# Optimization experiments

Measured on AMD Instinct MI355X. Metric: run time of the kernel, lower is better.

The kernel has to match this reference:

```python
import jax, jax.numpy as jnp
import numpy as np

HEADS = 16
DIMS = [64, 64, 64, 64]  # [d_att(Q), d_att(K), d_ff(V), d_ff(G)]
EPS = 1e-4
P_POW = 2


def _cdist(Q, K):
    # Euclidean pairwise distance via the norm expansion, like torch.cdist.
    # Q: [h, b, t, d], K: [h, b, t, d] -> [h, b, t, t]
    q2 = jnp.sum(Q * Q, axis=-1)  # [h, b, t]
    k2 = jnp.sum(K * K, axis=-1)  # [h, b, t]
    qk = jnp.einsum('hbtd,hbsd->hbts', Q, K)
    d2 = q2[..., :, None] + k2[..., None, :] - 2.0 * qk
    return jnp.sqrt(jnp.maximum(d2, 0.0))


def setup_inputs() -> dict:
    key = jax.random.key(0)
    ks = jax.random.split(key, 4)
    b, t, d_in = 2, 2048, 1024
    d_proj = HEADS * sum(DIMS)  # 4096
    X = jax.random.normal(ks[0], (b, t, d_in), dtype=jnp.float32)
    W_in = jax.random.normal(ks[1], (d_in, d_proj), dtype=jnp.float32) * (d_in ** -0.5)
    b_in = jnp.zeros((d_proj,), dtype=jnp.float32)
    W_out = jax.random.normal(ks[2], (HEADS * DIMS[2], d_in), dtype=jnp.float32) * ((HEADS * DIMS[2]) ** -0.5)
    b_out = jnp.zeros((d_in,), dtype=jnp.float32)
    return {"X": X, "W_in": W_in, "b_in": b_in, "W_out": W_out, "b_out": b_out}


def reference(X, W_in, b_in, W_out, b_out):
    b, t, _ = X.shape
    # multi-head input projection: [b,t,d_in] -> [h,b,t,sum(DIMS)] -> split
    P = X @ W_in + b_in                       # [b, t, h*sum(DIMS)]
    P = P.reshape(b, t, HEADS, sum(DIMS))
    P = jnp.transpose(P, (2, 0, 1, 3))        # [h, b, t, sum(DIMS)]
    splits = np.cumsum(DIMS)[:-1]
    Q, K, V, G = jnp.split(P, splits, axis=-1)
    # Shepard's attention: inverse-power-distance weights
    W = jnp.power(EPS + _cdist(Q, K), -P_POW)         # [h, b, t, t]
    W = W / (EPS + jnp.sum(W, axis=-1, keepdims=True))
    A = jnp.einsum('hbts,hbse->hbte', W, V)           # [h, b, t, e]
    H = G * A                                          # gating
    H = jnp.transpose(H, (1, 2, 0, 3)).reshape(b, t, HEADS * DIMS[2])
    return H @ W_out + b_out
```

## Files before the change

### kernel.cpp

```cpp
#include <hip/hip_runtime.h>
#include <hip/hip_bf16.h>
#include <cstdint>
#include <cstddef>

typedef __bf16 bf16_t;
typedef __attribute__((ext_vector_type(8))) __bf16 bf16x8;
typedef __attribute__((ext_vector_type(4))) float f32x4;
typedef __attribute__((ext_vector_type(16))) float f32x16;
typedef __attribute__((ext_vector_type(4))) unsigned int u32x4;

#define ATT_EPS 1e-4f

__device__ __forceinline__ f32x4 mfma_bf16(bf16x8 a, bf16x8 b, f32x4 c) {
  return __builtin_amdgcn_mfma_f32_16x16x32_bf16(a, b, c, 0, 0, 0);
}
__device__ __forceinline__ f32x16 mfma32(bf16x8 a, bf16x8 b, f32x16 c) {
  return __builtin_amdgcn_mfma_f32_32x32x16_bf16(a, b, c, 0, 0, 0);
}
__device__ __forceinline__ unsigned cvtpk_bf16(float lo, float hi) {
  unsigned r;
  asm("v_cvt_pk_bf16_f32 %0, %1, %2" : "=v"(r) : "v"(lo), "v"(hi));
  return r;
}

#define GLDS16(g, l)                                                          \
  __builtin_amdgcn_global_load_lds(                                           \
      (const __attribute__((address_space(1))) void*)(g),                     \
      (__attribute__((address_space(3))) void*)(l), 16, 0, 0)

__global__ __launch_bounds__(256) void cvt_x_kernel(
    const float* __restrict__ X, bf16_t* __restrict__ Xb, int n8) {
  int i = blockIdx.x * 256 + threadIdx.x;
  if (i >= n8) return;
  f32x4 a = ((const f32x4*)X)[i * 2 + 0];
  f32x4 b = ((const f32x4*)X)[i * 2 + 1];
  bf16x8 o;
  o[0] = (__bf16)a[0]; o[1] = (__bf16)a[1]; o[2] = (__bf16)a[2]; o[3] = (__bf16)a[3];
  o[4] = (__bf16)b[0]; o[5] = (__bf16)b[1]; o[6] = (__bf16)b[2]; o[7] = (__bf16)b[3];
  ((bf16x8*)Xb)[i] = o;
}

__global__ __launch_bounds__(256) void tcvt_kernel(
    const float* __restrict__ W, bf16_t* __restrict__ Wt, int R, int C) {
  __shared__ float T[64][65];
  int tx = threadIdx.x & 63, ty = threadIdx.x >> 6;
  int c0 = blockIdx.x * 64, r0 = blockIdx.y * 64;
#pragma unroll
  for (int i = 0; i < 16; ++i) {
    int rr = ty * 16 + i;
    T[rr][tx] = W[(size_t)(r0 + rr) * C + c0 + tx];
  }
  __syncthreads();
#pragma unroll
  for (int i = 0; i < 16; ++i) {
    int cc = ty * 16 + i;
    Wt[(size_t)(c0 + cc) * R + r0 + tx] = (bf16_t)T[tx][cc];
  }
}

template <int OUTF32, int FUSE>
__global__ __launch_bounds__(256, 2) void gemm_kernel(
    const bf16_t* __restrict__ A, const bf16_t* __restrict__ Bt,
    const float* __restrict__ bias, void* __restrict__ Cout,
    int M, int N, int K,
    float* __restrict__ Q2, bf16_t* __restrict__ K2E, bf16_t* __restrict__ VtG) {
  __shared__ bf16_t As[2][128 * 64];
  __shared__ bf16_t Bs[2][128 * 64];
  int tid = threadIdx.x, lane = tid & 63, wv = tid >> 6;
  int l15 = lane & 15, lhi = lane >> 4;
  int NT = N >> 7;
  int nwg = gridDim.x;
  int qq = nwg >> 3;
  int swz = (blockIdx.x & 7) * qq + (blockIdx.x >> 3);
  int tm = swz / NT, tn = swz % NT;
  int m0 = tm << 7, n0 = tn << 7;
  int wm = (wv >> 1) << 6, wn = (wv & 1) << 6;
  int KT = K >> 6;

  auto stage = [&](int buf, int kt) {
    int k0 = kt << 6;
#pragma unroll
    for (int s = 0; s < 4; ++s) {
      int t = s * 256 + tid;
      int row = t >> 3, u = t & 7;
      int cc = (u ^ (row & 7)) << 3;
      GLDS16(A + (size_t)(m0 + row) * K + k0 + cc, &As[buf][t * 8]);
    }
#pragma unroll
    for (int s = 0; s < 4; ++s) {
      int t = s * 256 + tid;
      int row = t >> 3, u = t & 7;
      int cc = (u ^ (row & 7)) << 3;
      GLDS16(Bt + (size_t)(n0 + row) * K + k0 + cc, &Bs[buf][t * 8]);
    }
  };

  f32x4 zero = {0.f, 0.f, 0.f, 0.f};
  f32x4 acc[4][4];
#pragma unroll
  for (int ms = 0; ms < 4; ++ms)
#pragma unroll
    for (int ns = 0; ns < 4; ++ns) acc[ms][ns] = zero;

  stage(0, 0);
  __syncthreads();
  int cur = 0;
  for (int kt = 0; kt < KT; ++kt) {
    if (kt + 1 < KT) stage(cur ^ 1, kt + 1);
#pragma unroll
    for (int ks = 0; ks < 2; ++ks) {
      bf16x8 af[4], bfr[4];
#pragma unroll
      for (int ms = 0; ms < 4; ++ms) {
        int row = wm + ms * 16 + l15;
        af[ms] = *(const bf16x8*)&As[cur][row * 64 + (((ks * 4 + lhi) ^ (row & 7)) << 3)];
      }
#pragma unroll
      for (int ns = 0; ns < 4; ++ns) {
        int col = wn + ns * 16 + l15;
        bfr[ns] = *(const bf16x8*)&Bs[cur][col * 64 + (((ks * 4 + lhi) ^ (col & 7)) << 3)];
      }
#pragma unroll
      for (int ms = 0; ms < 4; ++ms)
#pragma unroll
        for (int ns = 0; ns < 4; ++ns)
          acc[ms][ns] = mfma_bf16(af[ms], bfr[ns], acc[ms][ns]);
    }
    __syncthreads();
    cur ^= 1;
  }

#pragma unroll
  for (int ns = 0; ns < 4; ++ns) {
    float bv = bias[n0 + wn + ns * 16 + l15];
#pragma unroll
    for (int ms = 0; ms < 4; ++ms)
#pragma unroll
      for (int r = 0; r < 4; ++r) acc[ms][ns][r] += bv;
  }

  bool vg = FUSE && ((n0 >> 7) & 1);
  bool skipC = vg && (wn == 0);

  if (!skipC) {
#pragma unroll
    for (int ns = 0; ns < 4; ++ns) {
      int col = n0 + wn + ns * 16 + l15;
#pragma unroll
      for (int ms = 0; ms < 4; ++ms) {
        int rowb = m0 + wm + ms * 16 + lhi * 4;
#pragma unroll
        for (int r = 0; r < 4; ++r) {
          float v = acc[ms][ns][r];
          if (OUTF32)
            ((float*)Cout)[(size_t)(rowb + r) * N + col] = v;
          else
            ((bf16_t*)Cout)[(size_t)(rowb + r) * N + col] = (bf16_t)v;
        }
      }
    }
  }

  if (FUSE) {
    int h = n0 >> 8;
    if (!vg) {
#pragma unroll
      for (int ms = 0; ms < 4; ++ms)
#pragma unroll
        for (int r = 0; r < 4; ++r) {
          float s = 0.f;
#pragma unroll
          for (int ns = 0; ns < 4; ++ns) s += acc[ms][ns][r] * acc[ms][ns][r];
          s += __shfl_xor(s, 1);
          s += __shfl_xor(s, 2);
          s += __shfl_xor(s, 4);
          s += __shfl_xor(s, 8);
          if (l15 == 0) {
            int row = m0 + wm + ms * 16 + lhi * 4 + r;
            if (wn == 0) {
              Q2[h * 4096 + row] = s;
            } else {
              __bf16 kh = (__bf16)s;
              __bf16 kl = (__bf16)(s - (float)kh);
              bf16x8 rw;
              rw[0] = kh; rw[1] = kl;
              rw[2] = (__bf16)1.f; rw[3] = (__bf16)1.f;
              rw[4] = (__bf16)0.f; rw[5] = (__bf16)0.f;
              rw[6] = (__bf16)0.f; rw[7] = (__bf16)0.f;
              *(bf16x8*)&K2E[((size_t)h * 4096 + row) * 8] = rw;
            }
          }
        }
    } else {
      bf16_t* T = (bf16_t*)&As[0][0];
      if (wn == 0) {
#pragma unroll
        for (int ms = 0; ms < 4; ++ms)
#pragma unroll
          for (int ns = 0; ns < 4; ++ns)
#pragma unroll
            for (int r = 0; r < 4; ++r) {
              int row = wm + ms * 16 + lhi * 4 + r;
              int e = ns * 16 + l15;
              int prow = (row & ~15) | ((row & 3) | ((row & 4) << 1) | ((row & 8) >> 1));
              T[e * 136 + prow] = (bf16_t)acc[ms][ns][r];
            }
      }
      __syncthreads();
      int e = tid >> 2, c0 = (tid & 3) * 32;
      bf16_t* dst = VtG + (size_t)(h * 64 + e) * 4096 + m0 + c0;
#pragma unroll
      for (int j = 0; j < 4; ++j)
        *(bf16x8*)&dst[j * 8] = *(bf16x8*)&T[e * 136 + c0 + j * 8];
    }
  }
}

__global__ __launch_bounds__(512, 4) void attn_kernel(
    const bf16_t* __restrict__ P, const bf16_t* __restrict__ VtG,
    const float* __restrict__ Q2, const bf16_t* __restrict__ K2E,
    bf16_t* __restrict__ H) {
  __shared__ union Smem {
    struct {
      bf16_t Ks[2][128 * 64];
      bf16_t Vts[2][64 * 128];
      bf16_t K2e[2][128 * 8];
    } l;
    float Comb[4][64][33];
  } sm;
  __shared__ float invLds[4][32];

  int tid = threadIdx.x, lane = tid & 63, wv = tid >> 6;
  int l31 = lane & 31, hi = lane >> 5, hi4 = hi * 4;
  int qw = wv & 3, sw = wv >> 2;
  int sOff = sw * 64;
  int swz = (blockIdx.x & 7) * 64 + (blockIdx.x >> 3);
  int hb = swz >> 4, qt = swz & 15;
  int h = hb >> 1, b = hb & 1;
  int rowbase = b * 2048;
  const bf16_t* Pq = P + (size_t)rowbase * 4096 + h * 256;
  const bf16_t* Pk = Pq + 64;
  const bf16_t* Pg = Pq + 192;
  const bf16_t* Vg = VtG + (size_t)h * 64 * 4096 + rowbase;
  const float* Q2g = Q2 + h * 4096 + rowbase;
  const bf16_t* K2Eg = K2E + ((size_t)h * 4096 + rowbase) * 8;
  int q0 = qt * 128 + qw * 32;

  auto stageKV = [&](int buf, int s0) {
#pragma unroll
    for (int s4 = 0; s4 < 2; ++s4) {
      int t = s4 * 512 + tid;
      int row = t >> 3, u = t & 7;
      int cc = (u ^ (row & 7)) << 3;
      GLDS16(Pk + (size_t)(s0 + row) * 4096 + cc, &sm.l.Ks[buf][t * 8]);
    }
#pragma unroll
    for (int s4 = 0; s4 < 2; ++s4) {
      int t = s4 * 512 + tid;
      int row = t >> 4, u = t & 15;
      int cc = (u ^ (row & 7)) << 3;
      GLDS16(Vg + (size_t)row * 4096 + s0 + cc, &sm.l.Vts[buf][t * 8]);
    }
    if (tid < 128)
      GLDS16(K2Eg + (size_t)(s0 + tid) * 8, &sm.l.K2e[buf][tid * 8]);
  };

  bf16x8 qm[4];
#pragma unroll
  for (int db = 0; db < 4; ++db) {
    bf16x8 q = *(const bf16x8*)(Pq + (size_t)(q0 + l31) * 4096 + db * 16 + hi * 8);
    u32x4 u = *(u32x4*)&q;
    u = (u ^ 0x80008000u) + 0x00800080u;
    qm[db] = *(bf16x8*)&u;
  }
  float q2s = Q2g[q0 + l31];
  __bf16 q2h = (__bf16)q2s;
  __bf16 q2l = (__bf16)(q2s - (float)q2h);
  bf16x8 qmE;
  qmE[0] = hi ? (__bf16)0.f : (__bf16)1.f;
  qmE[1] = qmE[0];
  qmE[2] = hi ? (__bf16)0.f : q2h;
  qmE[3] = hi ? (__bf16)0.f : q2l;
  qmE[4] = (__bf16)0.f; qmE[5] = (__bf16)0.f;
  qmE[6] = (__bf16)0.f; qmE[7] = (__bf16)0.f;

  f32x16 zero16;
#pragma unroll
  for (int r = 0; r < 16; ++r) zero16[r] = 0.f;

  f32x16 nacc0 = zero16, nacc1 = zero16;
  float dacc0 = 0.f, dacc1 = 0.f;

  stageKV(0, 0);
  __syncthreads();

  for (int st = 0; st < 16; ++st) {
    int cur = st & 1;
    int s0 = st * 128;
    if (st + 1 < 16) stageKV(cur ^ 1, s0 + 128);

    const bf16_t* KsC = sm.l.Ks[cur];
    const bf16_t* VtC = sm.l.Vts[cur];
    const bf16_t* K2eC = sm.l.K2e[cur];
#pragma unroll
    for (int sb = 0; sb < 2; ++sb) {
      int sbase = sOff + sb * 32;
      int srow = sbase + l31;
      bf16x8 ke = *(const bf16x8*)&K2eC[srow * 8];
      u32x4 keu = *(u32x4*)&ke;
      u32x4 kz;
      kz[0] = hi ? 0u : keu[0];
      kz[1] = hi ? 0u : keu[1];
      kz[2] = 0u; kz[3] = 0u;
      bf16x8 kfE = *(bf16x8*)&kz;
      f32x16 D = mfma32(kfE, qmE, zero16);
#pragma unroll
      for (int db = 0; db < 4; ++db) {
        bf16x8 kf = *(const bf16x8*)&KsC[srow * 64 + (((db * 2 + hi) ^ (srow & 7)) << 3)];
        D = mfma32(kf, qm[db], D);
      }
      float p[16];
#pragma unroll
      for (int r = 0; r < 16; ++r) {
        float w = __builtin_amdgcn_rcpf(fmaxf(D[r], 1e-12f));
        if (r & 1) dacc1 += w; else dacc0 += w;
        p[r] = w;
      }
      u32x4 w0v = {cvtpk_bf16(p[0], p[1]), cvtpk_bf16(p[2], p[3]),
                   cvtpk_bf16(p[4], p[5]), cvtpk_bf16(p[6], p[7])};
      u32x4 w1v = {cvtpk_bf16(p[8], p[9]), cvtpk_bf16(p[10], p[11]),
                   cvtpk_bf16(p[12], p[13]), cvtpk_bf16(p[14], p[15])};
      bf16x8 pa0 = *(bf16x8*)&w0v;
      bf16x8 pa1 = *(bf16x8*)&w1v;
      int e = l31;
      int ciB = (sOff >> 3) + sb * 4;
      bf16x8 vb00 = *(const bf16x8*)&VtC[e * 128 + (((ciB + 0 + hi) ^ (e & 7)) << 3)];
      bf16x8 vb01 = *(const bf16x8*)&VtC[(e + 32) * 128 + (((ciB + 0 + hi) ^ ((e + 32) & 7)) << 3)];
      bf16x8 vb10 = *(const bf16x8*)&VtC[e * 128 + (((ciB + 2 + hi) ^ (e & 7)) << 3)];
      bf16x8 vb11 = *(const bf16x8*)&VtC[(e + 32) * 128 + (((ciB + 2 + hi) ^ ((e + 32) & 7)) << 3)];
      nacc0 = mfma32(pa0, vb00, nacc0);
      nacc1 = mfma32(pa0, vb01, nacc1);
      nacc0 = mfma32(pa1, vb10, nacc0);
      nacc1 = mfma32(pa1, vb11, nacc1);
    }
    __syncthreads();
  }

  if (sw == 1) {
#pragma unroll
    for (int r = 0; r < 16; ++r) {
      sm.Comb[qw][lane][r] = nacc0[r];
      sm.Comb[qw][lane][16 + r] = nacc1[r];
    }
    sm.Comb[qw][lane][32] = dacc0 + dacc1;
  }
  __syncthreads();
  if (sw == 0) {
    float dacc = dacc0 + dacc1 + sm.Comb[qw][lane][32];
#pragma unroll
    for (int r = 0; r < 16; ++r) {
      nacc0[r] += sm.Comb[qw][lane][r];
      nacc1[r] += sm.Comb[qw][lane][16 + r];
    }
    dacc += __shfl_xor(dacc, 32);
    float inv = __builtin_amdgcn_rcpf(ATT_EPS + dacc);
    if (lane < 32) invLds[qw][l31] = inv;
    __builtin_amdgcn_s_waitcnt(0);
#pragma unroll
    for (int r = 0; r < 16; ++r) {
      int q = (r & 3) + 8 * (r >> 2) + hi4;
      int tq = q0 + q;
      float iv = invLds[qw][q];
      float g0 = (float)Pg[(size_t)tq * 4096 + l31];
      float g1 = (float)Pg[(size_t)tq * 4096 + 32 + l31];
      H[(size_t)(rowbase + tq) * 1024 + h * 64 + l31] = (bf16_t)(g0 * nacc0[r] * iv);
      H[(size_t)(rowbase + tq) * 1024 + h * 64 + 32 + l31] = (bf16_t)(g1 * nacc1[r] * iv);
    }
  }
}

extern "C" void kernel_launch(void* const* d_in, const int* in_sizes, int n_in,
                              void* d_out, int out_size, void* d_ws, size_t ws_size,
                              hipStream_t stream) {
  const float* X     = (const float*)d_in[0];
  const float* W_in  = (const float*)d_in[1];
  const float* b_in  = (const float*)d_in[2];
  const float* W_out = (const float*)d_in[3];
  const float* b_out = (const float*)d_in[4];

  char* ws = (char*)d_ws;
  bf16_t* Xb  = (bf16_t*)(ws);
  bf16_t* WbT = (bf16_t*)(ws + ((size_t)8  << 20));
  bf16_t* WoT = (bf16_t*)(ws + ((size_t)16 << 20));
  bf16_t* Pb  = (bf16_t*)(ws + ((size_t)18 << 20));
  bf16_t* Hb  = (bf16_t*)(ws + ((size_t)50 << 20));
  float*  Q2  = (float*) (ws + ((size_t)58 << 20));
  bf16_t* VtG = (bf16_t*)d_out;
  bf16_t* K2E = (bf16_t*)((char*)d_out + ((size_t)8 << 20));

  cvt_x_kernel<<<2048, 256, 0, stream>>>(X, Xb, 4096 * 1024 / 8);
  tcvt_kernel<<<dim3(64, 16), 256, 0, stream>>>(W_in, WbT, 1024, 4096);
  tcvt_kernel<<<dim3(16, 16), 256, 0, stream>>>(W_out, WoT, 1024, 1024);
  gemm_kernel<0, 1><<<1024, 256, 0, stream>>>(Xb, WbT, b_in, Pb, 4096, 4096, 1024,
                                              Q2, K2E, VtG);
  attn_kernel<<<512, 512, 0, stream>>>(Pb, VtG, Q2, K2E, Hb);
  gemm_kernel<1, 0><<<256, 256, 0, stream>>>(Hb, WoT, b_out, d_out, 4096, 1024, 1024,
                                             nullptr, nullptr, nullptr);
}
```

Baseline: 133.3 us.

## Fuse X fp32-to-bf16 conversion into input GEMM and merge weight transposes

Removes the separate X conversion kernel: the input-projection GEMM now loads fp32 X tiles into registers, converts them to bf16 and writes them into swizzled LDS after the MFMA loop, overlapping the global load with compute. The two weight transpose-convert launches are merged into one launch. This drops two kernel launches and the round trip of the bf16 X buffer through memory. In exchange, the GEMM reads twice as many bytes for A, each block repeats the conversion for its tile, and the register staging adds pressure under launch_bounds(256,2).

```diff
diff --git a/kernel.cpp b/kernel.cpp
--- a/kernel.cpp
+++ b/kernel.cpp
@@ -28,23 +28,23 @@
       (const __attribute__((address_space(1))) void*)(g),                     \
       (__attribute__((address_space(3))) void*)(l), 16, 0, 0)
 
-__global__ __launch_bounds__(256) void cvt_x_kernel(
-    const float* __restrict__ X, bf16_t* __restrict__ Xb, int n8) {
-  int i = blockIdx.x * 256 + threadIdx.x;
-  if (i >= n8) return;
-  f32x4 a = ((const f32x4*)X)[i * 2 + 0];
-  f32x4 b = ((const f32x4*)X)[i * 2 + 1];
-  bf16x8 o;
-  o[0] = (__bf16)a[0]; o[1] = (__bf16)a[1]; o[2] = (__bf16)a[2]; o[3] = (__bf16)a[3];
-  o[4] = (__bf16)b[0]; o[5] = (__bf16)b[1]; o[6] = (__bf16)b[2]; o[7] = (__bf16)b[3];
-  ((bf16x8*)Xb)[i] = o;
-}
-
-__global__ __launch_bounds__(256) void tcvt_kernel(
-    const float* __restrict__ W, bf16_t* __restrict__ Wt, int R, int C) {
+__global__ __launch_bounds__(256) void tcvt2_kernel(
+    const float* __restrict__ Wi, bf16_t* __restrict__ WiT,
+    const float* __restrict__ Wo, bf16_t* __restrict__ WoT) {
   __shared__ float T[64][65];
   int tx = threadIdx.x & 63, ty = threadIdx.x >> 6;
-  int c0 = blockIdx.x * 64, r0 = blockIdx.y * 64;
+  const float* W;
+  bf16_t* Wt;
+  int c0, r0, R, C;
+  if (blockIdx.y < 16) {
+    W = Wi; Wt = WiT; R = 1024; C = 4096;
+    c0 = blockIdx.x * 64; r0 = blockIdx.y * 64;
+  } else {
+    int idx = (blockIdx.y - 16) * 64 + blockIdx.x;
+    if (idx >= 256) return;
+    W = Wo; Wt = WoT; R = 1024; C = 1024;
+    c0 = (idx & 15) * 64; r0 = (idx >> 4) * 64;
+  }
 #pragma unroll
   for (int i = 0; i < 16; ++i) {
     int rr = ty * 16 + i;
@@ -58,14 +58,16 @@
   }
 }
 
-template <int OUTF32, int FUSE>
+template <int OUTF32, int FUSE, int AF32>
 __global__ __launch_bounds__(256, 2) void gemm_kernel(
-    const bf16_t* __restrict__ A, const bf16_t* __restrict__ Bt,
+    const void* __restrict__ Av, const bf16_t* __restrict__ Bt,
     const float* __restrict__ bias, void* __restrict__ Cout,
     int M, int N, int K,
     float* __restrict__ Q2, bf16_t* __restrict__ K2E, bf16_t* __restrict__ VtG) {
   __shared__ bf16_t As[2][128 * 64];
   __shared__ bf16_t Bs[2][128 * 64];
+  const bf16_t* A = (const bf16_t*)Av;
+  const float* Af = (const float*)Av;
   int tid = threadIdx.x, lane = tid & 63, wv = tid >> 6;
   int l15 = lane & 15, lhi = lane >> 4;
   int NT = N >> 7;
@@ -77,15 +79,38 @@
   int wm = (wv >> 1) << 6, wn = (wv & 1) << 6;
   int KT = K >> 6;
 
-  auto stage = [&](int buf, int kt) {
+  f32x4 ar[4][2];
+
+  auto stageA = [&](int buf, int kt) {
     int k0 = kt << 6;
 #pragma unroll
     for (int s = 0; s < 4; ++s) {
       int t = s * 256 + tid;
       int row = t >> 3, u = t & 7;
       int cc = (u ^ (row & 7)) << 3;
-      GLDS16(A + (size_t)(m0 + row) * K + k0 + cc, &As[buf][t * 8]);
-    }
+      if (AF32) {
+        const float* src = Af + (size_t)(m0 + row) * K + k0 + cc;
+        ar[s][0] = *(const f32x4*)src;
+        ar[s][1] = *(const f32x4*)(src + 4);
+      } else {
+        GLDS16(A + (size_t)(m0 + row) * K + k0 + cc, &As[buf][t * 8]);
+      }
+    }
+  };
+  auto stageA_write = [&](int buf) {
+#pragma unroll
+    for (int s = 0; s < 4; ++s) {
+      int t = s * 256 + tid;
+      u32x4 w;
+      w[0] = cvtpk_bf16(ar[s][0][0], ar[s][0][1]);
+      w[1] = cvtpk_bf16(ar[s][0][2], ar[s][0][3]);
+      w[2] = cvtpk_bf16(ar[s][1][0], ar[s][1][1]);
+      w[3] = cvtpk_bf16(ar[s][1][2], ar[s][1][3]);
+      *(u32x4*)&As[buf][t * 8] = w;
+    }
+  };
+  auto stageB = [&](int buf, int kt) {
+    int k0 = kt << 6;
 #pragma unroll
     for (int s = 0; s < 4; ++s) {
       int t = s * 256 + tid;
@@ -102,11 +127,16 @@
 #pragma unroll
     for (int ns = 0; ns < 4; ++ns) acc[ms][ns] = zero;
 
-  stage(0, 0);
+  stageA(0, 0);
+  stageB(0, 0);
+  if (AF32) stageA_write(0);
   __syncthreads();
   int cur = 0;
   for (int kt = 0; kt < KT; ++kt) {
-    if (kt + 1 < KT) stage(cur ^ 1, kt + 1);
+    if (kt + 1 < KT) {
+      stageA(cur ^ 1, kt + 1);
+      stageB(cur ^ 1, kt + 1);
+    }
 #pragma unroll
     for (int ks = 0; ks < 2; ++ks) {
       bf16x8 af[4], bfr[4];
@@ -126,6 +156,7 @@
         for (int ns = 0; ns < 4; ++ns)
           acc[ms][ns] = mfma_bf16(af[ms], bfr[ns], acc[ms][ns]);
     }
+    if (AF32 && kt + 1 < KT) stageA_write(cur ^ 1);
     __syncthreads();
     cur ^= 1;
   }
@@ -389,7 +420,6 @@
   const float* b_out = (const float*)d_in[4];
 
   char* ws = (char*)d_ws;
-  bf16_t* Xb  = (bf16_t*)(ws);
   bf16_t* WbT = (bf16_t*)(ws + ((size_t)8  << 20));
   bf16_t* WoT = (bf16_t*)(ws + ((size_t)16 << 20));
   bf16_t* Pb  = (bf16_t*)(ws + ((size_t)18 << 20));
@@ -398,12 +428,10 @@
   bf16_t* VtG = (bf16_t*)d_out;
   bf16_t* K2E = (bf16_t*)((char*)d_out + ((size_t)8 << 20));
 
-  cvt_x_kernel<<<2048, 256, 0, stream>>>(X, Xb, 4096 * 1024 / 8);
-  tcvt_kernel<<<dim3(64, 16), 256, 0, stream>>>(W_in, WbT, 1024, 4096);
-  tcvt_kernel<<<dim3(16, 16), 256, 0, stream>>>(W_out, WoT, 1024, 1024);
-  gemm_kernel<0, 1><<<1024, 256, 0, stream>>>(Xb, WbT, b_in, Pb, 4096, 4096, 1024,
-                                              Q2, K2E, VtG);
+  tcvt2_kernel<<<dim3(64, 20), 256, 0, stream>>>(W_in, WbT, W_out, WoT);
+  gemm_kernel<0, 1, 1><<<1024, 256, 0, stream>>>(X, WbT, b_in, Pb, 4096, 4096, 1024,
+                                                 Q2, K2E, VtG);
   attn_kernel<<<512, 512, 0, stream>>>(Pb, VtG, Q2, K2E, Hb);
-  gemm_kernel<1, 0><<<256, 256, 0, stream>>>(Hb, WoT, b_out, d_out, 4096, 1024, 1024,
-                                             nullptr, nullptr, nullptr);
-}
+  gemm_kernel<1, 0, 0><<<256, 256, 0, stream>>>(Hb, WoT, b_out, d_out, 4096, 1024, 1024,
+                                                nullptr, nullptr, nullptr);
+}
```

Result: slower. 138.2 us (+3.7%).

## Halve attention KV tile to raise occupancy and merge weight transpose launches

Applied to the files above, without the earlier changes.

The attention kernel now stages 64 keys per iteration instead of 128, halving its LDS footprint, and raises the launch-bounds hint from 4 to 8 blocks. The key loop runs twice as many iterations with one sub-block per wave. The aim is more resident waves per CU to hide latency, at the cost of more barriers and more frequent staging. Separately, the two weight transpose-convert launches are merged into one kernel to save a launch.

```diff
diff --git a/kernel.cpp b/kernel.cpp
--- a/kernel.cpp
+++ b/kernel.cpp
@@ -40,11 +40,23 @@
   ((bf16x8*)Xb)[i] = o;
 }
 
-__global__ __launch_bounds__(256) void tcvt_kernel(
-    const float* __restrict__ W, bf16_t* __restrict__ Wt, int R, int C) {
+__global__ __launch_bounds__(256) void tcvt2_kernel(
+    const float* __restrict__ Wi, bf16_t* __restrict__ WiT,
+    const float* __restrict__ Wo, bf16_t* __restrict__ WoT) {
   __shared__ float T[64][65];
   int tx = threadIdx.x & 63, ty = threadIdx.x >> 6;
-  int c0 = blockIdx.x * 64, r0 = blockIdx.y * 64;
+  const float* W;
+  bf16_t* Wt;
+  int c0, r0, R, C;
+  if (blockIdx.y < 16) {
+    W = Wi; Wt = WiT; R = 1024; C = 4096;
+    c0 = blockIdx.x * 64; r0 = blockIdx.y * 64;
+  } else {
+    int idx = (blockIdx.y - 16) * 64 + blockIdx.x;
+    if (idx >= 256) return;
+    W = Wo; Wt = WoT; R = 1024; C = 1024;
+    c0 = (idx & 15) * 64; r0 = (idx >> 4) * 64;
+  }
 #pragma unroll
   for (int i = 0; i < 16; ++i) {
     int rr = ty * 16 + i;
@@ -216,15 +228,15 @@
   }
 }
 
-__global__ __launch_bounds__(512, 4) void attn_kernel(
+__global__ __launch_bounds__(512, 8) void attn_kernel(
     const bf16_t* __restrict__ P, const bf16_t* __restrict__ VtG,
     const float* __restrict__ Q2, const bf16_t* __restrict__ K2E,
     bf16_t* __restrict__ H) {
   __shared__ union Smem {
     struct {
-      bf16_t Ks[2][128 * 64];
-      bf16_t Vts[2][64 * 128];
-      bf16_t K2e[2][128 * 8];
+      bf16_t Ks[2][64 * 64];
+      bf16_t Vts[2][64 * 64];
+      bf16_t K2e[2][64 * 8];
     } l;
     float Comb[4][64][33];
   } sm;
@@ -233,7 +245,7 @@
   int tid = threadIdx.x, lane = tid & 63, wv = tid >> 6;
   int l31 = lane & 31, hi = lane >> 5, hi4 = hi * 4;
   int qw = wv & 3, sw = wv >> 2;
-  int sOff = sw * 64;
+  int sOff = sw * 32;
   int swz = (blockIdx.x & 7) * 64 + (blockIdx.x >> 3);
   int hb = swz >> 4, qt = swz & 15;
   int h = hb >> 1, b = hb & 1;
@@ -247,21 +259,17 @@
   int q0 = qt * 128 + qw * 32;
 
   auto stageKV = [&](int buf, int s0) {
-#pragma unroll
-    for (int s4 = 0; s4 < 2; ++s4) {
-      int t = s4 * 512 + tid;
-      int row = t >> 3, u = t & 7;
+    {
+      int row = tid >> 3, u = tid & 7;
       int cc = (u ^ (row & 7)) << 3;
-      GLDS16(Pk + (size_t)(s0 + row) * 4096 + cc, &sm.l.Ks[buf][t * 8]);
-    }
-#pragma unroll
-    for (int s4 = 0; s4 < 2; ++s4) {
-      int t = s4 * 512 + tid;
-      int row = t >> 4, u = t & 15;
+      GLDS16(Pk + (size_t)(s0 + row) * 4096 + cc, &sm.l.Ks[buf][tid * 8]);
+    }
+    {
+      int row = tid >> 3, u = tid & 7;
       int cc = (u ^ (row & 7)) << 3;
-      GLDS16(Vg + (size_t)row * 4096 + s0 + cc, &sm.l.Vts[buf][t * 8]);
-    }
-    if (tid < 128)
+      GLDS16(Vg + (size_t)row * 4096 + s0 + cc, &sm.l.Vts[buf][tid * 8]);
+    }
+    if (tid < 64)
       GLDS16(K2Eg + (size_t)(s0 + tid) * 8, &sm.l.K2e[buf][tid * 8]);
   };
 
@@ -294,18 +302,16 @@
   stageKV(0, 0);
   __syncthreads();
 
-  for (int st = 0; st < 16; ++st) {
+  for (int st = 0; st < 32; ++st) {
     int cur = st & 1;
-    int s0 = st * 128;
-    if (st + 1 < 16) stageKV(cur ^ 1, s0 + 128);
+    int s0 = st * 64;
+    if (st + 1 < 32) stageKV(cur ^ 1, s0 + 64);
 
     const bf16_t* KsC = sm.l.Ks[cur];
     const bf16_t* VtC = sm.l.Vts[cur];
     const bf16_t* K2eC = sm.l.K2e[cur];
-#pragma unroll
-    for (int sb = 0; sb < 2; ++sb) {
-      int sbase = sOff + sb * 32;
-      int srow = sbase + l31;
+    {
+      int srow = sOff + l31;
       bf16x8 ke = *(const bf16x8*)&K2eC[srow * 8];
       u32x4 keu = *(u32x4*)&ke;
       u32x4 kz;
@@ -333,11 +339,11 @@
       bf16x8 pa0 = *(bf16x8*)&w0v;
       bf16x8 pa1 = *(bf16x8*)&w1v;
       int e = l31;
-      int ciB = (sOff >> 3) + sb * 4;
-      bf16x8 vb00 = *(const bf16x8*)&VtC[e * 128 + (((ciB + 0 + hi) ^ (e & 7)) << 3)];
-      bf16x8 vb01 = *(const bf16x8*)&VtC[(e + 32) * 128 + (((ciB + 0 + hi) ^ ((e + 32) & 7)) << 3)];
-      bf16x8 vb10 = *(const bf16x8*)&VtC[e * 128 + (((ciB + 2 + hi) ^ (e & 7)) << 3)];
-      bf16x8 vb11 = *(const bf16x8*)&VtC[(e + 32) * 128 + (((ciB + 2 + hi) ^ ((e + 32) & 7)) << 3)];
+      int ciB = sw * 4;
+      bf16x8 vb00 = *(const bf16x8*)&VtC[e * 64 + (((ciB + 0 + hi) ^ (e & 7)) << 3)];
+      bf16x8 vb01 = *(const bf16x8*)&VtC[(e + 32) * 64 + (((ciB + 0 + hi) ^ ((e + 32) & 7)) << 3)];
+      bf16x8 vb10 = *(const bf16x8*)&VtC[e * 64 + (((ciB + 2 + hi) ^ (e & 7)) << 3)];
+      bf16x8 vb11 = *(const bf16x8*)&VtC[(e + 32) * 64 + (((ciB + 2 + hi) ^ ((e + 32) & 7)) << 3)];
       nacc0 = mfma32(pa0, vb00, nacc0);
       nacc1 = mfma32(pa0, vb01, nacc1);
       nacc0 = mfma32(pa1, vb10, nacc0);
@@ -399,8 +405,7 @@
   bf16_t* K2E = (bf16_t*)((char*)d_out + ((size_t)8 << 20));
 
   cvt_x_kernel<<<2048, 256, 0, stream>>>(X, Xb, 4096 * 1024 / 8);
-  tcvt_kernel<<<dim3(64, 16), 256, 0, stream>>>(W_in, WbT, 1024, 4096);
-  tcvt_kernel<<<dim3(16, 16), 256, 0, stream>>>(W_out, WoT, 1024, 1024);
+  tcvt2_kernel<<<dim3(64, 20), 256, 0, stream>>>(W_in, WbT, W_out, WoT);
   gemm_kernel<0, 1><<<1024, 256, 0, stream>>>(Xb, WbT, b_in, Pb, 4096, 4096, 1024,
                                               Q2, K2E, VtG);
   attn_kernel<<<512, 512, 0, stream>>>(Pb, VtG, Q2, K2E, Hb);
```

Result: slower. 253.2 us (+90.0%).
